# Optimization experiments

Hardware: AMD Instinct MI355X
Metric: run time of the kernel (lower is better)

## Reference

```python
import jax, jax.numpy as jnp
import numpy as np

D_MODEL = 1024
D_KEY = 64
N_HEADS = 16
B, T = 4, 2048


def setup_inputs() -> dict:
    key = jax.random.key(0)
    ks = jax.random.split(key, 12)
    s = 0.02
    return {
        "keys": jax.random.normal(ks[0], (B, T, D_MODEL), jnp.float32),
        "queries": jax.random.normal(ks[1], (B, T, D_MODEL), jnp.float32),
        "values": jax.random.normal(ks[2], (B, T, D_MODEL), jnp.float32),
        "pad_mask": jnp.ones((B, T), jnp.int32),
        "WK_w": jax.random.normal(ks[3], (D_KEY * N_HEADS, D_MODEL), jnp.float32) * s,
        "WK_b": jnp.zeros((D_KEY * N_HEADS,), jnp.float32),
        "WQ_w": jax.random.normal(ks[4], (D_KEY * N_HEADS, D_MODEL), jnp.float32) * s,
        "WQ_b": jnp.zeros((D_KEY * N_HEADS,), jnp.float32),
        "WV_w": jax.random.normal(ks[5], (D_KEY * N_HEADS, D_MODEL), jnp.float32) * s,
        "WV_b": jnp.zeros((D_KEY * N_HEADS,), jnp.float32),
        "WO_w": jax.random.normal(ks[6], (D_MODEL, D_KEY * N_HEADS), jnp.float32) * s,
        "WO_b": jnp.zeros((D_MODEL,), jnp.float32),
    }


def reference(keys, queries, values, pad_mask, WK_w, WK_b, WQ_w, WQ_b, WV_w, WV_b, WO_w, WO_b):
    # NOTE: the original torch module calls masked_fill (non-inplace) and discards
    # the result, so neither the causal mask nor pad_mask has any effect. We
    # faithfully reproduce that: no masking. pad_mask is an unused constant.
    batch, time = keys.shape[:2]
    k = keys @ WK_w.T + WK_b      # [B,T,H*dk]
    q = queries @ WQ_w.T + WQ_b
    v = values @ WV_w.T + WV_b

    def split_heads(x):
        return x.reshape(batch, time, N_HEADS, D_KEY).transpose(0, 2, 1, 3)  # [B,H,T,dk]

    k, q, v = split_heads(k), split_heads(q), split_heads(v)
    # scores[t,s] = k_t . q_s / sqrt(d_key)  (K and Q swapped, as in source)
    scores = jnp.einsum("bhtd,bhsd->bhts", k, q) / jnp.sqrt(jnp.float32(D_KEY))
    attn = jax.nn.softmax(scores, axis=-1)             # [B,H,T,T]
    ctx = jnp.einsum("bhts,bhsd->bhtd", attn, v)       # [B,H,T,dk]
    ctx = ctx.transpose(0, 2, 1, 3).reshape(batch, time, N_HEADS * D_KEY)
    return ctx @ WO_w.T + WO_b
```

## Files before the change

kernel.cpp:

```cpp
#include <hip/hip_runtime.h>

typedef unsigned short u16;
typedef unsigned int u32;
typedef __attribute__((ext_vector_type(8))) short short8;
typedef __attribute__((ext_vector_type(4))) float f32x4;

__device__ __forceinline__ u16 f2bf(float f) {
    unsigned int u = __float_as_uint(f);
    u += 0x7fffu + ((u >> 16) & 1u);
    return (u16)(u >> 16);
}

__device__ __forceinline__ u32 pack_trunc(float a, float b) {
    return __builtin_amdgcn_perm(__float_as_uint(b), __float_as_uint(a), 0x07060302u);
}

__device__ __forceinline__ void gload16(const u16* g, const u16* l) {
    __builtin_amdgcn_global_load_lds(
        (const __attribute__((address_space(1))) unsigned int*)g,
        (__attribute__((address_space(3))) unsigned int*)l, 16, 0, 0);
}

__global__ __launch_bounds__(256) void cast_all(const float* __restrict__ k,
                                                const float* __restrict__ q,
                                                const float* __restrict__ v,
                                                const float* __restrict__ wk,
                                                const float* __restrict__ wq,
                                                const float* __restrict__ wv,
                                                const float* __restrict__ wo,
                                                u16* __restrict__ Xk, u16* __restrict__ Xq,
                                                u16* __restrict__ Xv, u16* __restrict__ Wk,
                                                u16* __restrict__ Wq, u16* __restrict__ Wv,
                                                u16* __restrict__ Wo) {
    size_t i = ((size_t)blockIdx.x * 256 + threadIdx.x) * 8;
    const float* src; u16* dst; size_t off;
    if (i < 25165824) {
        int r = (int)(i >> 23); off = i & 8388607;
        src = r == 0 ? k : (r == 1 ? q : v);
        dst = r == 0 ? Xk : (r == 1 ? Xq : Xv);
    } else {
        size_t j = i - 25165824;
        int r = (int)(j >> 20); off = j & 1048575;
        src = r == 0 ? wk : (r == 1 ? wq : (r == 2 ? wv : wo));
        dst = r == 0 ? Wk : (r == 1 ? Wq : (r == 2 ? Wv : Wo));
    }
    float4 a = *(const float4*)(src + off);
    float4 b = *(const float4*)(src + off + 4);
    union { u16 h[8]; uint4 u; } r8;
    r8.h[0] = f2bf(a.x); r8.h[1] = f2bf(a.y); r8.h[2] = f2bf(a.z); r8.h[3] = f2bf(a.w);
    r8.h[4] = f2bf(b.x); r8.h[5] = f2bf(b.y); r8.h[6] = f2bf(b.z); r8.h[7] = f2bf(b.w);
    *(uint4*)(dst + off) = r8.u;
}


__global__ __launch_bounds__(256) void gemm_qkv(const u16* __restrict__ Xk,
                                                const u16* __restrict__ Xq,
                                                const u16* __restrict__ Xv,
                                                const u16* __restrict__ Wk,
                                                const u16* __restrict__ Wq,
                                                const u16* __restrict__ Wv,
                                                const float* __restrict__ bK,
                                                const float* __restrict__ bQ,
                                                const float* __restrict__ bV,
                                                u16* __restrict__ Kbh,
                                                u16* __restrict__ Qbh,
                                                u16* __restrict__ Vtg,
                                                float kscale) {
    __shared__ u16 sA[128 * 64];
    __shared__ u16 sB[128 * 64];
    const int f = blockIdx.x;
    const int z = f >> 9;
    const int r9 = f & 511;
    const int i_idx = (r9 & 7) | (((r9 >> 6) & 7) << 3);
    const int j_idx = (r9 >> 3) & 7;

    const u16* X = z == 0 ? Xk : (z == 1 ? Xq : Xv);
    const u16* W = z == 0 ? Wk : (z == 1 ? Wq : Wv);
    const float* bias = z == 0 ? bK : (z == 1 ? bQ : bV);
    u16* out = z == 0 ? Kbh : (z == 1 ? Qbh : Vtg);
    const float scale = z == 0 ? kscale : 1.0f;

    const int tid  = threadIdx.x;
    const int wave = tid >> 6, lane = tid & 63;
    const int quad = lane >> 4, l16 = lane & 15;
    const int wm = wave & 1, wn = wave >> 1;
    const int i0 = i_idx * 128, j0 = j_idx * 128;

    const int r = tid >> 3;
    const int sg = (tid & 7) ^ (r & 7);
    const u16* gA = X + (size_t)(i0 + r) * 1024 + sg * 8;
    const u16* gB = W + (size_t)(j0 + r) * 1024 + sg * 8;
    u16* dA = sA + wave * 512;
    u16* dB = sB + wave * 512;
    const int sx = l16 & 7;

    f32x4 acc[4][4];
    #pragma unroll
    for (int mt = 0; mt < 4; mt++)
        #pragma unroll
        for (int nt = 0; nt < 4; nt++) acc[mt][nt] = (f32x4){0.f, 0.f, 0.f, 0.f};

    for (int kk = 0; kk < 1024; kk += 64) {
        __syncthreads();
        gload16(gA + kk,         dA);
        gload16(gA + kk + 32768, dA + 2048);
        gload16(gA + kk + 65536, dA + 4096);
        gload16(gA + kk + 98304, dA + 6144);
        gload16(gB + kk,         dB);
        gload16(gB + kk + 32768, dB + 2048);
        gload16(gB + kk + 65536, dB + 4096);
        gload16(gB + kk + 98304, dB + 6144);
        __syncthreads();
        short8 bf[4][2];
        #pragma unroll
        for (int nt = 0; nt < 4; nt++)
            #pragma unroll
            for (int kh = 0; kh < 2; kh++)
                bf[nt][kh] = *(const short8*)&sB[(wn * 64 + nt * 16 + l16) * 64 +
                                                 ((kh * 4 + quad) ^ sx) * 8];
        #pragma unroll
        for (int mt = 0; mt < 4; mt++) {
            const int arow = (wm * 64 + mt * 16 + l16) * 64;
            short8 a0 = *(const short8*)&sA[arow + ((quad) ^ sx) * 8];
            short8 a1 = *(const short8*)&sA[arow + ((4 + quad) ^ sx) * 8];
            #pragma unroll
            for (int nt = 0; nt < 4; nt++) {
                acc[mt][nt] = __builtin_amdgcn_mfma_f32_16x16x32_bf16(a0, bf[nt][0], acc[mt][nt], 0, 0, 0);
                acc[mt][nt] = __builtin_amdgcn_mfma_f32_16x16x32_bf16(a1, bf[nt][1], acc[mt][nt], 0, 0, 0);
            }
        }
    }

    #pragma unroll
    for (int mt = 0; mt < 4; mt++) {
        #pragma unroll
        for (int nt = 0; nt < 4; nt++) {
            int j = j0 + wn * 64 + nt * 16 + l16;
            float bj = bias[j];
            #pragma unroll
            for (int rr = 0; rr < 4; rr++) {
                int i = i0 + wm * 64 + mt * 16 + quad * 4 + rr;
                float v = (acc[mt][nt][rr] + bj) * scale;
                int b = i >> 11, t = i & 2047;
                int h = j >> 6,  dd = j & 63;
                size_t idx;
                if (z == 2) idx = (((size_t)(b * 16 + h)) * 64 + dd) * 2048 + t;
                else        idx = (((size_t)(b * 16 + h)) * 2048 + t) * 64 + dd;
                out[idx] = f2bf(v);
            }
        }
    }
}

__global__ __launch_bounds__(256) void gemm_out(const u16* __restrict__ X,
                                                const u16* __restrict__ W,
                                                const float* __restrict__ bias,
                                                float* __restrict__ out) {
    __shared__ u16 sA[128 * 64];
    __shared__ u16 sB[64 * 64];
    const int f = blockIdx.x;
    const int j_idx = (f >> 3) & 15;
    const int i_idx = (f & 7) | ((f >> 7) << 3);
    const int tid  = threadIdx.x;
    const int wave = tid >> 6, lane = tid & 63;
    const int quad = lane >> 4, l16 = lane & 15;
    const int wm = wave & 1, wn = wave >> 1;
    const int i0 = i_idx * 128, j0 = j_idx * 64;

    const int r = tid >> 3;
    const int sg = (tid & 7) ^ (r & 7);
    const u16* gA = X + (size_t)(i0 + r) * 1024 + sg * 8;
    const u16* gB = W + (size_t)(j0 + r) * 1024 + sg * 8;
    u16* dA = sA + wave * 512;
    u16* dB = sB + wave * 512;
    const int sx = l16 & 7;

    f32x4 acc[4][2];
    #pragma unroll
    for (int mt = 0; mt < 4; mt++) {
        acc[mt][0] = (f32x4){0.f, 0.f, 0.f, 0.f};
        acc[mt][1] = (f32x4){0.f, 0.f, 0.f, 0.f};
    }

    for (int kk = 0; kk < 1024; kk += 64) {
        __syncthreads();
        gload16(gA + kk,         dA);
        gload16(gA + kk + 32768, dA + 2048);
        gload16(gA + kk + 65536, dA + 4096);
        gload16(gA + kk + 98304, dA + 6144);
        gload16(gB + kk,         dB);
        gload16(gB + kk + 32768, dB + 2048);
        __syncthreads();
        short8 bf[2][2];
        #pragma unroll
        for (int nt = 0; nt < 2; nt++)
            #pragma unroll
            for (int kh = 0; kh < 2; kh++)
                bf[nt][kh] = *(const short8*)&sB[(wn * 32 + nt * 16 + l16) * 64 +
                                                 ((kh * 4 + quad) ^ sx) * 8];
        #pragma unroll
        for (int mt = 0; mt < 4; mt++) {
            const int arow = (wm * 64 + mt * 16 + l16) * 64;
            short8 a0 = *(const short8*)&sA[arow + ((quad) ^ sx) * 8];
            short8 a1 = *(const short8*)&sA[arow + ((4 + quad) ^ sx) * 8];
            #pragma unroll
            for (int nt = 0; nt < 2; nt++) {
                acc[mt][nt] = __builtin_amdgcn_mfma_f32_16x16x32_bf16(a0, bf[nt][0], acc[mt][nt], 0, 0, 0);
                acc[mt][nt] = __builtin_amdgcn_mfma_f32_16x16x32_bf16(a1, bf[nt][1], acc[mt][nt], 0, 0, 0);
            }
        }
    }

    #pragma unroll
    for (int mt = 0; mt < 4; mt++) {
        #pragma unroll
        for (int nt = 0; nt < 2; nt++) {
            int j = j0 + wn * 32 + nt * 16 + l16;
            float bj = bias[j];
            #pragma unroll
            for (int rr = 0; rr < 4; rr++) {
                int i = i0 + wm * 64 + mt * 16 + quad * 4 + rr;
                out[(size_t)i * 1024 + j] = acc[mt][nt][rr] + bj;
            }
        }
    }
}

__global__ __launch_bounds__(256, 2) void attn_kernel(const u16* __restrict__ Kbh,
                                                      const u16* __restrict__ Qbh,
                                                      const u16* __restrict__ Vtg,
                                                      u16* __restrict__ ctx) {
    __shared__ u16 sQ[2 * 64 * 64];
    __shared__ u16 sVt[2 * 64 * 64];
    __shared__ u16 sP[4 * 2 * 16 * 64];
    const int f = blockIdx.x;
    const int bh = (f & 7) | ((f >> 6) << 3);
    const int tx = (f >> 3) & 7;
    const int tid  = threadIdx.x;
    const int wave = tid >> 6, lane = tid & 63;
    const int quad = lane >> 4, l16 = lane & 15;
    const int sx = l16 & 7;
    const int tw = tx * 256 + wave * 64;
    const size_t base = (size_t)bh * 2048 * 64;

    short8 bk[4][2];
    #pragma unroll
    for (int g = 0; g < 4; g++) {
        const u16* kr = Kbh + base + (size_t)(tw + g * 16 + l16) * 64 + quad * 8;
        bk[g][0] = *(const short8*)kr;
        bk[g][1] = *(const short8*)(kr + 32);
    }
    const short8 ones = {0x3F80, 0x3F80, 0x3F80, 0x3F80, 0x3F80, 0x3F80, 0x3F80, 0x3F80};

    f32x4 accO[4][4];
    #pragma unroll
    for (int g = 0; g < 4; g++)
        #pragma unroll
        for (int dt = 0; dt < 4; dt++) accO[g][dt] = (f32x4){0.f, 0.f, 0.f, 0.f};
    f32x4 accL[4];
    #pragma unroll
    for (int g = 0; g < 4; g++) accL[g] = (f32x4){0.f, 0.f, 0.f, 0.f};

    const int srow = tid >> 2, seg = tid & 3;
    const int s7 = srow & 7;
    const int st0 = ((2 * seg)     ^ s7) * 8;
    const int st1 = ((2 * seg + 1) ^ s7) * 8;
    u16* sPw = sP + wave * 2048;

    const u16* gQ = Qbh + base + (size_t)srow * 64 + seg * 16;
    const u16* gV = Vtg + ((size_t)bh * 64 + srow) * 2048 + seg * 16;

    uint4 q0 = ((const uint4*)gQ)[0], q1 = ((const uint4*)gQ)[1];
    uint4 v0 = ((const uint4*)gV)[0], v1 = ((const uint4*)gV)[1];

    for (int it = 0; it < 32; it++) {
        u16* dQ = sQ  + (it & 1) * 4096;
        u16* dV = sVt + (it & 1) * 4096;
        *(uint4*)&dQ[srow * 64 + st0] = q0;
        *(uint4*)&dQ[srow * 64 + st1] = q1;
        *(uint4*)&dV[srow * 64 + st0] = v0;
        *(uint4*)&dV[srow * 64 + st1] = v1;
        if (it + 1 < 32) {
            const int sn = (it + 1) * 64;
            const uint4* nq = (const uint4*)(gQ + (size_t)sn * 64);
            const uint4* nv = (const uint4*)(gV + sn);
            q0 = nq[0]; q1 = nq[1];
            v0 = nv[0]; v1 = nv[1];
        }
        asm volatile("s_waitcnt lgkmcnt(0)" ::: "memory");
        __builtin_amdgcn_s_barrier();
        __builtin_amdgcn_sched_barrier(0);

        short8 aq[4][2], av[2][4];
        #pragma unroll
        for (int nt = 0; nt < 4; nt++)
            #pragma unroll
            for (int kh = 0; kh < 2; kh++)
                aq[nt][kh] = *(const short8*)&dQ[(nt * 16 + l16) * 64 +
                                                 ((kh * 4 + quad) ^ sx) * 8];
        #pragma unroll
        for (int kk = 0; kk < 2; kk++)
            #pragma unroll
            for (int dt = 0; dt < 4; dt++)
                av[kk][dt] = *(const short8*)&dV[(dt * 16 + l16) * 64 +
                                                 ((kk * 4 + quad) ^ sx) * 8];

        #pragma unroll
        for (int g = 0; g < 4; g++) {
            f32x4 aS[4];
            __builtin_amdgcn_s_setprio(1);
            #pragma unroll
            for (int nt = 0; nt < 4; nt++) {
                f32x4 s = __builtin_amdgcn_mfma_f32_16x16x32_bf16(aq[nt][0], bk[g][0],
                            (f32x4){0.f, 0.f, 0.f, 0.f}, 0, 0, 0);
                aS[nt] = __builtin_amdgcn_mfma_f32_16x16x32_bf16(aq[nt][1], bk[g][1], s, 0, 0, 0);
            }
            __builtin_amdgcn_s_setprio(0);
            u16* pb = sPw + (g & 1) * 1024;
            #pragma unroll
            for (int nt = 0; nt < 4; nt++) {
                float p0 = __builtin_amdgcn_exp2f(aS[nt][0]);
                float p1 = __builtin_amdgcn_exp2f(aS[nt][1]);
                float p2 = __builtin_amdgcn_exp2f(aS[nt][2]);
                float p3 = __builtin_amdgcn_exp2f(aS[nt][3]);
                uint2 pk = { pack_trunc(p0, p1), pack_trunc(p2, p3) };
                *(uint2*)&pb[l16 * 64 + ((nt * 4 + quad) ^ (sx << 1)) * 4] = pk;
            }
            __builtin_amdgcn_s_setprio(1);
            #pragma unroll
            for (int kk = 0; kk < 2; kk++) {
                short8 bp = *(const short8*)&pb[l16 * 64 +
                                                ((kk * 8 + quad * 2) ^ (sx << 1)) * 4];
                accL[g] = __builtin_amdgcn_mfma_f32_16x16x32_bf16(ones, bp, accL[g], 0, 0, 0);
                #pragma unroll
                for (int dt = 0; dt < 4; dt++)
                    accO[g][dt] = __builtin_amdgcn_mfma_f32_16x16x32_bf16(av[kk][dt], bp, accO[g][dt], 0, 0, 0);
            }
            __builtin_amdgcn_s_setprio(0);
        }
    }

    const int b = bh >> 4, h = bh & 15;
    #pragma unroll
    for (int g = 0; g < 4; g++) {
        float inv = 1.f / accL[g][0];
        int t = tw + g * 16 + l16;
        u16* orow = ctx + ((size_t)(b * 2048 + t)) * 1024 + h * 64;
        #pragma unroll
        for (int dt = 0; dt < 4; dt++) {
            union { u16 h4[4]; uint2 u; } o;
            #pragma unroll
            for (int rr = 0; rr < 4; rr++) o.h4[rr] = f2bf(accO[g][dt][rr] * inv);
            *(uint2*)&orow[dt * 16 + quad * 4] = o.u;
        }
    }
}

extern "C" void kernel_launch(void* const* d_in, const int* in_sizes, int n_in,
                              void* d_out, int out_size, void* d_ws, size_t ws_size,
                              hipStream_t stream) {
    const float* keys    = (const float*)d_in[0];
    const float* queries = (const float*)d_in[1];
    const float* values  = (const float*)d_in[2];
    const float* WKb = (const float*)d_in[5];
    const float* WQb = (const float*)d_in[7];
    const float* WVb = (const float*)d_in[9];
    const float* WOb = (const float*)d_in[11];

    char* ws = (char*)d_ws;
    const size_t MB = 1 << 20;
    u16* Kbh = (u16*)(ws + 0 * MB);
    u16* Qbh = (u16*)(ws + 16 * MB);
    u16* Vtg = (u16*)(ws + 32 * MB);
    u16* Xk  = (u16*)(ws + 48 * MB);
    u16* Xq  = (u16*)(ws + 64 * MB);
    u16* Xv  = (u16*)(ws + 80 * MB);
    u16* Wk  = (u16*)(ws + 96 * MB);
    u16* Wq  = (u16*)(ws + 98 * MB);
    u16* Wv  = (u16*)(ws + 100 * MB);
    u16* Wo  = (u16*)(ws + 102 * MB);
    u16* ctx = (u16*)(ws + 48 * MB);

    cast_all<<<14336, 256, 0, stream>>>(keys, queries, values,
                                        (const float*)d_in[4], (const float*)d_in[6],
                                        (const float*)d_in[8], (const float*)d_in[10],
                                        Xk, Xq, Xv, Wk, Wq, Wv, Wo);

    const float kscale = 1.4426950408889634f * 0.125f;
    gemm_qkv<<<1536, 256, 0, stream>>>(Xk, Xq, Xv, Wk, Wq, Wv,
                                       WKb, WQb, WVb, Kbh, Qbh, Vtg, kscale);

    attn_kernel<<<512, 256, 0, stream>>>(Kbh, Qbh, Vtg, ctx);

    gemm_out<<<1024, 256, 0, stream>>>(ctx, Wo, WOb, (float*)d_out);
}
```

Measured before the change: 330.2 us.

## Fuse activation fp32-to-bf16 cast into QKV GEMM A-tile load

Removes the separate cast pass over keys/queries/values. The QKV GEMM now loads fp32 activations into registers, converts them with packed bf16 conversion and writes them to swizzled LDS, prefetching the next k-tile during compute. Only the weights are still cast in a smaller kernel. This avoids writing and re-reading the bf16 activation copies, at the cost of doubled A-tile global bytes and register pressure inside the GEMM.

After: 337.3 us. 2.1% more time.

```diff
diff --git a/kernel.cpp b/kernel.cpp
--- a/kernel.cpp
+++ b/kernel.cpp
@@ -15,35 +15,28 @@
     return __builtin_amdgcn_perm(__float_as_uint(b), __float_as_uint(a), 0x07060302u);
 }
 
+__device__ __forceinline__ u32 cvt_pk_bf16(float a, float b) {
+    u32 r;
+    asm volatile("v_cvt_pk_bf16_f32 %0, %1, %2" : "=v"(r) : "v"(a), "v"(b));
+    return r;
+}
+
 __device__ __forceinline__ void gload16(const u16* g, const u16* l) {
     __builtin_amdgcn_global_load_lds(
         (const __attribute__((address_space(1))) unsigned int*)g,
         (__attribute__((address_space(3))) unsigned int*)l, 16, 0, 0);
 }
 
-__global__ __launch_bounds__(256) void cast_all(const float* __restrict__ k,
-                                                const float* __restrict__ q,
-                                                const float* __restrict__ v,
-                                                const float* __restrict__ wk,
-                                                const float* __restrict__ wq,
-                                                const float* __restrict__ wv,
-                                                const float* __restrict__ wo,
-                                                u16* __restrict__ Xk, u16* __restrict__ Xq,
-                                                u16* __restrict__ Xv, u16* __restrict__ Wk,
-                                                u16* __restrict__ Wq, u16* __restrict__ Wv,
-                                                u16* __restrict__ Wo) {
+__global__ __launch_bounds__(256) void cast_w(const float* __restrict__ wk,
+                                              const float* __restrict__ wq,
+                                              const float* __restrict__ wv,
+                                              const float* __restrict__ wo,
+                                              u16* __restrict__ Wk, u16* __restrict__ Wq,
+                                              u16* __restrict__ Wv, u16* __restrict__ Wo) {
     size_t i = ((size_t)blockIdx.x * 256 + threadIdx.x) * 8;
-    const float* src; u16* dst; size_t off;
-    if (i < 25165824) {
-        int r = (int)(i >> 23); off = i & 8388607;
-        src = r == 0 ? k : (r == 1 ? q : v);
-        dst = r == 0 ? Xk : (r == 1 ? Xq : Xv);
-    } else {
-        size_t j = i - 25165824;
-        int r = (int)(j >> 20); off = j & 1048575;
-        src = r == 0 ? wk : (r == 1 ? wq : (r == 2 ? wv : wo));
-        dst = r == 0 ? Wk : (r == 1 ? Wq : (r == 2 ? Wv : Wo));
-    }
+    int r = (int)(i >> 20); size_t off = i & 1048575;
+    const float* src = r == 0 ? wk : (r == 1 ? wq : (r == 2 ? wv : wo));
+    u16* dst        = r == 0 ? Wk : (r == 1 ? Wq : (r == 2 ? Wv : Wo));
     float4 a = *(const float4*)(src + off);
     float4 b = *(const float4*)(src + off + 4);
     union { u16 h[8]; uint4 u; } r8;
@@ -53,9 +46,9 @@
 }
 
 
-__global__ __launch_bounds__(256) void gemm_qkv(const u16* __restrict__ Xk,
-                                                const u16* __restrict__ Xq,
-                                                const u16* __restrict__ Xv,
+__global__ __launch_bounds__(256) void gemm_qkv(const float* __restrict__ Xk,
+                                                const float* __restrict__ Xq,
+                                                const float* __restrict__ Xv,
                                                 const u16* __restrict__ Wk,
                                                 const u16* __restrict__ Wq,
                                                 const u16* __restrict__ Wv,
@@ -74,8 +67,8 @@
     const int i_idx = (r9 & 7) | (((r9 >> 6) & 7) << 3);
     const int j_idx = (r9 >> 3) & 7;
 
-    const u16* X = z == 0 ? Xk : (z == 1 ? Xq : Xv);
-    const u16* W = z == 0 ? Wk : (z == 1 ? Wq : Wv);
+    const float* X = z == 0 ? Xk : (z == 1 ? Xq : Xv);
+    const u16*   W = z == 0 ? Wk : (z == 1 ? Wq : Wv);
     const float* bias = z == 0 ? bK : (z == 1 ? bQ : bV);
     u16* out = z == 0 ? Kbh : (z == 1 ? Qbh : Vtg);
     const float scale = z == 0 ? kscale : 1.0f;
@@ -86,11 +79,13 @@
     const int wm = wave & 1, wn = wave >> 1;
     const int i0 = i_idx * 128, j0 = j_idx * 128;
 
+    const float* gAf = X + (size_t)(i0 + (tid >> 4)) * 1024 + (tid & 15) * 4;
+    u16* dAw = sA + (tid >> 4) * 64 +
+               ((((tid & 15) >> 1) ^ ((tid >> 4) & 7)) * 8) + (tid & 1) * 4;
+
     const int r = tid >> 3;
     const int sg = (tid & 7) ^ (r & 7);
-    const u16* gA = X + (size_t)(i0 + r) * 1024 + sg * 8;
     const u16* gB = W + (size_t)(j0 + r) * 1024 + sg * 8;
-    u16* dA = sA + wave * 512;
     u16* dB = sB + wave * 512;
     const int sx = l16 & 7;
 
@@ -100,17 +95,29 @@
         #pragma unroll
         for (int nt = 0; nt < 4; nt++) acc[mt][nt] = (f32x4){0.f, 0.f, 0.f, 0.f};
 
+    float4 ar[8];
+    #pragma unroll
+    for (int j = 0; j < 8; j++) ar[j] = *(const float4*)(gAf + (size_t)j * 16384);
+
     for (int kk = 0; kk < 1024; kk += 64) {
         __syncthreads();
-        gload16(gA + kk,         dA);
-        gload16(gA + kk + 32768, dA + 2048);
-        gload16(gA + kk + 65536, dA + 4096);
-        gload16(gA + kk + 98304, dA + 6144);
+        #pragma unroll
+        for (int j = 0; j < 8; j++) {
+            uint2 p;
+            p.x = cvt_pk_bf16(ar[j].x, ar[j].y);
+            p.y = cvt_pk_bf16(ar[j].z, ar[j].w);
+            *(uint2*)(dAw + j * 1024) = p;
+        }
         gload16(gB + kk,         dB);
         gload16(gB + kk + 32768, dB + 2048);
         gload16(gB + kk + 65536, dB + 4096);
         gload16(gB + kk + 98304, dB + 6144);
         __syncthreads();
+        if (kk + 64 < 1024) {
+            #pragma unroll
+            for (int j = 0; j < 8; j++)
+                ar[j] = *(const float4*)(gAf + (size_t)j * 16384 + kk + 64);
+        }
         short8 bf[4][2];
         #pragma unroll
         for (int nt = 0; nt < 4; nt++)
@@ -372,22 +379,18 @@
     u16* Kbh = (u16*)(ws + 0 * MB);
     u16* Qbh = (u16*)(ws + 16 * MB);
     u16* Vtg = (u16*)(ws + 32 * MB);
-    u16* Xk  = (u16*)(ws + 48 * MB);
-    u16* Xq  = (u16*)(ws + 64 * MB);
-    u16* Xv  = (u16*)(ws + 80 * MB);
+    u16* ctx = (u16*)(ws + 48 * MB);
     u16* Wk  = (u16*)(ws + 96 * MB);
     u16* Wq  = (u16*)(ws + 98 * MB);
     u16* Wv  = (u16*)(ws + 100 * MB);
     u16* Wo  = (u16*)(ws + 102 * MB);
-    u16* ctx = (u16*)(ws + 48 * MB);
-
-    cast_all<<<14336, 256, 0, stream>>>(keys, queries, values,
-                                        (const float*)d_in[4], (const float*)d_in[6],
-                                        (const float*)d_in[8], (const float*)d_in[10],
-                                        Xk, Xq, Xv, Wk, Wq, Wv, Wo);
+
+    cast_w<<<2048, 256, 0, stream>>>((const float*)d_in[4], (const float*)d_in[6],
+                                     (const float*)d_in[8], (const float*)d_in[10],
+                                     Wk, Wq, Wv, Wo);
 
     const float kscale = 1.4426950408889634f * 0.125f;
-    gemm_qkv<<<1536, 256, 0, stream>>>(Xk, Xq, Xv, Wk, Wq, Wv,
+    gemm_qkv<<<1536, 256, 0, stream>>>(keys, queries, values, Wk, Wq, Wv,
                                        WKb, WQb, WVb, Kbh, Qbh, Vtg, kscale);
 
     attn_kernel<<<512, 256, 0, stream>>>(Kbh, Qbh, Vtg, ctx);
```
